# Kernel optimization log

Hardware: AMD Instinct MI355X
Metric: run time of the kernel (lower is better)

Reference implementation:

```python
import jax, jax.numpy as jnp
import numpy as np

B, H, W, Q, E, M, K, WIN = 4, 192, 192, 160, 96, 96, 4, 7
NO_ELECTRON_WEIGHT = 0.1


def _bce_logits(x, z):
    # binary_cross_entropy_with_logits, elementwise: softplus(x) - x*z
    return jnp.logaddexp(0.0, x) - x * z


def setup_inputs() -> dict:
    key = jax.random.key(0)
    ks = jax.random.split(key, 11)
    is_electron_logit = jax.random.normal(ks[0], (B * Q,), jnp.float32)
    true_segmap = jax.random.uniform(ks[1], (B, H, W, E), jnp.float32)
    binary_mask_logits = jax.random.normal(ks[2], (B, H, W, Q), jnp.float32)
    portion_logits = jax.random.normal(ks[3], (B, H, W, Q), jnp.float32)
    # keep incidence points away from borders so the 7x7 window stays in-bounds
    incidence_points = jax.random.uniform(ks[4], (B, E, 2), jnp.float32) * (H - 8) + 4.0
    positions = jax.random.uniform(ks[5], (B, Q, 2), jnp.float32) * H
    a = jax.random.normal(ks[6], (B, Q, 3), jnp.float32)
    l00 = jax.nn.softplus(a[..., 0]) + 0.1
    l11 = jax.nn.softplus(a[..., 2]) + 0.1
    l10 = 0.5 * a[..., 1]
    zero = jnp.zeros_like(l00)
    chol = jnp.stack([jnp.stack([l00, zero], -1), jnp.stack([l10, l11], -1)], -2)  # [B,Q,2,2] lower-tri
    occupancy_logits = jax.random.normal(ks[7], (B, H, W, K), jnp.float32)
    occupancy_true = jax.random.randint(ks[8], (B, H, W), 0, K, jnp.int32)
    qkeys = jax.random.split(ks[9], B)
    matched_q = jnp.stack([jax.random.permutation(k, Q)[:M] for k in qkeys]).astype(jnp.int32)
    ekeys = jax.random.split(ks[10], B)
    matched_e = jnp.stack([jax.random.permutation(k, E) for k in ekeys]).astype(jnp.int32)
    return dict(is_electron_logit=is_electron_logit, true_segmap=true_segmap,
                binary_mask_logits=binary_mask_logits, portion_logits=portion_logits,
                incidence_points=incidence_points, positions=positions, chol=chol,
                occupancy_logits=occupancy_logits, occupancy_true=occupancy_true,
                matched_q=matched_q, matched_e=matched_e)


def reference(is_electron_logit, true_segmap, binary_mask_logits, portion_logits,
              incidence_points, positions, chol, occupancy_logits, occupancy_true,
              matched_q, matched_e):
    # ---- class loss (weighted BCE over flat per-query logits) ----
    labels = jnp.zeros((B * Q,), is_electron_logit.dtype)
    glob = (jnp.arange(B)[:, None] * Q + matched_q).reshape(-1)
    labels = labels.at[glob].set(1.0)
    weights = jnp.where(labels > 0, 1.0, NO_ELECTRON_WEIGHT).astype(is_electron_logit.dtype)
    class_loss = jnp.mean(weights * _bce_logits(is_electron_logit, labels))

    # ---- reorder segmentation maps to matched order (_reorder_segmentation_map) ----
    true_r = jnp.take_along_axis(true_segmap, matched_e[:, None, None, :], axis=3)        # [B,H,W,M]
    bin_r = jnp.take_along_axis(binary_mask_logits, matched_q[:, None, None, :], axis=3)  # [B,H,W,M]
    por_r = jnp.take_along_axis(portion_logits, matched_q[:, None, None, :], axis=3)      # [B,H,W,M]

    # ---- mask BCE on 7x7 windows around floor(matched incidence point) ----
    pts_r = jnp.take_along_axis(incidence_points, matched_e[..., None], axis=1)  # [B,M,2]
    pix = jnp.floor(pts_r).astype(jnp.int32)
    half = WIN // 2
    dr = jnp.arange(-half, half + 1)
    rows = pix[..., 0][:, :, None, None] + dr[None, None, :, None]  # [B,M,7,1]
    cols = pix[..., 1][:, :, None, None] + dr[None, None, None, :]  # [B,M,1,7]
    bi = jnp.arange(B)[:, None, None, None]
    mi = jnp.arange(M)[None, :, None, None]
    tv = true_r[bi, rows, cols, mi]  # [B,M,7,7]
    lg = bin_r[bi, rows, cols, mi]
    bce_loss = jnp.mean(_bce_logits(lg, tv))

    # ---- dice loss (softmax over matched-electron dim) ----
    portion = jax.nn.softmax(por_r, axis=-1)
    num = jnp.sum(2.0 * true_r * portion, axis=(1, 2, 3))
    den = jnp.sum(true_r + portion, axis=(1, 2, 3))
    dice_loss = jnp.mean(1.0 - (num + 1.0) / (den + 1.0))

    # ---- distance NLL (2D MVN with lower-tri scale) ----
    centers_r = jnp.take_along_axis(positions, matched_q[..., None], axis=1)       # [B,M,2]
    chol_r = jnp.take_along_axis(chol, matched_q[..., None, None], axis=1)         # [B,M,2,2]
    d = pts_r - centers_r
    z0 = d[..., 0] / chol_r[..., 0, 0]
    z1 = (d[..., 1] - chol_r[..., 1, 0] * z0) / chol_r[..., 1, 1]
    nll = 0.5 * (z0 * z0 + z1 * z1) + jnp.log(2.0 * jnp.pi) \
          + jnp.log(chol_r[..., 0, 0]) + jnp.log(chol_r[..., 1, 1])
    nll = jnp.where(jnp.isinf(nll), 1e7, nll)
    nll_loss = jnp.mean(nll)

    # ---- occupancy loss (per-pixel electron-count cross-entropy) ----
    logp = jax.nn.log_softmax(occupancy_logits, axis=-1)
    occ_loss = -jnp.mean(jnp.take_along_axis(logp, occupancy_true[..., None], axis=-1))

    # loss_weights all 1.0 (defaults); dot(weights, terms)
    return class_loss + bce_loss + dice_loss + nll_loss + occ_loss
```

## Files before the change

### kernel.cpp

```cpp
#include <hip/hip_runtime.h>
#include <math.h>

#define B_ 4
#define H_ 192
#define W_ 192
#define Q_ 160
#define E_ 96
#define M_ 96
#define HW_ (H_ * W_)
#define NPIX_ (B_ * HW_)
#define TPIX 8
#define TILES_PER_BLK 18
#define NDICE 1024
#define NSMALL 962
#define NBUCKET 64
#define WS_NUM0 4
#define WS_TS0  260
#define WS_TOTAL 516

#define POR_BYTES (TPIX * Q_ * 4)
#define TRU_BYTES (TPIX * E_ * 4)
#define TILE_BYTES (POR_BYTES + TRU_BYTES)
#define POR_F (TPIX * Q_)

__device__ __forceinline__ void stage16(const void* g, void* l) {
    __builtin_amdgcn_global_load_lds(
        (const __attribute__((address_space(1))) void*)g,
        (__attribute__((address_space(3))) void*)l, 16, 0, 0);
}

template <int CTRL, int RMASK>
__device__ __forceinline__ float dpp_add_step(float x) {
    int v = __builtin_amdgcn_update_dpp(0, __float_as_int(x), CTRL, RMASK, 0xF, false);
    return x + __int_as_float(v);
}
__device__ __forceinline__ float wave_sum63(float x) {
    x = dpp_add_step<0x111, 0xF>(x);
    x = dpp_add_step<0x112, 0xF>(x);
    x = dpp_add_step<0x114, 0xF>(x);
    x = dpp_add_step<0x118, 0xF>(x);
    x = dpp_add_step<0x142, 0xA>(x);
    x = dpp_add_step<0x143, 0xC>(x);
    return x;
}

__device__ __forceinline__ float waveSumAll(float v) {
    for (int m = 32; m > 0; m >>= 1) v += __shfl_xor(v, m, 64);
    return v;
}

__device__ __forceinline__ float softplusf(float x) {
    return fmaxf(x, 0.f) + log1pf(__expf(-fabsf(x)));
}

__global__ __launch_bounds__(256) void fused_kernel(
    const float* __restrict__ logit,
    const float* __restrict__ trueseg,
    const float* __restrict__ binlog,
    const float* __restrict__ por,
    const float* __restrict__ inc,
    const float* __restrict__ pos,
    const float* __restrict__ chol,
    const float* __restrict__ occlog,
    const int* __restrict__ occtrue,
    const int* __restrict__ mqall,
    const int* __restrict__ meall,
    float* __restrict__ ws)
{
    __shared__ float tilebuf[2 * TILE_BYTES / 4];
    const int tid  = threadIdx.x;
    const int lane = tid & 63;
    const int wid  = tid >> 6;
    const int blk  = blockIdx.x;

    if (blk < NDICE) {
        const int b = blk >> 8;
        const int slot = blk & 255;
        const bool hi = lane < 32;
        const int* mq = mqall + b * M_;
        const int* me = meall + b * M_;
        const int mqa = mq[lane];
        const int mea = me[lane];
        int mqb = 0, meb = 0;
        if (hi) { mqb = mq[64 + lane]; meb = me[64 + lane]; }
        const char* porb = (const char*)(por + (size_t)b * HW_ * Q_);
        const char* trb  = (const char*)(trueseg + (size_t)b * HW_ * E_);

        float an = 0.f;
        float at = 0.f;

        {
            const int p0 = slot * TPIX;
            const char* gp = porb + (size_t)p0 * (Q_ * 4);
            const char* gt = trb  + (size_t)p0 * (E_ * 4);
            #pragma unroll
            for (int i = 0; i < 2; ++i) {
                const int off = i * 4096 + wid * 1024;
                const char* src = (off < POR_BYTES) ? (gp + off)
                                                    : (gt + (off - POR_BYTES));
                stage16(src + lane * 16, (char*)tilebuf + off);
            }
        }

        int bufsel = 0;
        for (int t = 0; t < TILES_PER_BLK; ++t) {
            __syncthreads();
            if (t + 1 < TILES_PER_BLK) {
                const int p0 = (slot + (t + 1) * 256) * TPIX;
                const char* gp = porb + (size_t)p0 * (Q_ * 4);
                const char* gt = trb  + (size_t)p0 * (E_ * 4);
                const int nb = bufsel ^ 1;
                #pragma unroll
                for (int i = 0; i < 2; ++i) {
                    const int off = i * 4096 + wid * 1024;
                    const char* src = (off < POR_BYTES) ? (gp + off)
                                                        : (gt + (off - POR_BYTES));
                    stage16(src + lane * 16, (char*)tilebuf + nb * TILE_BYTES + off);
                }
            }
            const float* pl = tilebuf + bufsel * (TILE_BYTES / 4);
            const float* tl = pl + POR_F;
            #pragma unroll
            for (int k = 0; k < 2; ++k) {
                const int pix = wid * 2 + k;
                float p0v = pl[pix * Q_ + mqa];
                float t0  = tl[pix * E_ + mea];
                float e1 = 0.f, se1 = 0.f, t1 = 0.f;
                if (hi) {
                    float p1 = pl[pix * Q_ + mqb];
                    t1 = tl[pix * E_ + meb];
                    e1 = __expf(p1);
                    se1 = t1 * e1;
                }
                float e0 = __expf(p0v);
                float s  = wave_sum63(e0 + e1);
                float se = wave_sum63(t0 * e0 + se1);
                an += __fdividef(se, s);
                at += t0 + t1;
            }
            bufsel ^= 1;
        }
        float atr = wave_sum63(at);
        if (lane == 63) {
            int bucket = blk & (NBUCKET - 1);
            atomicAdd(&ws[WS_NUM0 + bucket * 4 + b], 2.f * an);
            atomicAdd(&ws[WS_TS0  + bucket * 4 + b], atr);
        }
    } else {
        float* lab = tilebuf;
        const int s = blk - NDICE;
        float acc = 0.f;
        if (s == 0) {
            for (int i = tid; i < B_ * Q_; i += 256) lab[i] = 0.f;
            __syncthreads();
            for (int i = tid; i < B_ * M_; i += 256) {
                int b = i / M_;
                lab[b * Q_ + mqall[i]] = 1.f;
            }
            __syncthreads();
            for (int i = tid; i < B_ * Q_; i += 256) {
                float x = logit[i];
                float z = lab[i];
                float w = z > 0.f ? 1.f : 0.1f;
                acc += w * (softplusf(x) - x * z);
            }
            float wsum = wave_sum63(acc);
            if (lane == 63) atomicAdd(&ws[0], wsum);
        } else if (s == 1) {
            for (int i = tid; i < B_ * M_; i += 256) {
                int b = i / M_;
                int qi = mqall[i];
                int ei = meall[i];
                float px = inc[(b * E_ + ei) * 2 + 0];
                float py = inc[(b * E_ + ei) * 2 + 1];
                float cx = pos[(b * Q_ + qi) * 2 + 0];
                float cy = pos[(b * Q_ + qi) * 2 + 1];
                const float* ch = chol + (size_t)(b * Q_ + qi) * 4;
                float l00 = ch[0], l10 = ch[2], l11 = ch[3];
                float d0 = px - cx, d1 = py - cy;
                float z0 = d0 / l00;
                float z1 = (d1 - l10 * z0) / l11;
                float nll = 0.5f * (z0 * z0 + z1 * z1) + 1.837877066409345f
                            + logf(l00) + logf(l11);
                if (isinf(nll)) nll = 1e7f;
                acc += nll;
            }
            float wsum = wave_sum63(acc);
            if (lane == 63) atomicAdd(&ws[2], wsum);
        } else if (s < 386) {
            int idx = s - 2;
            int b = idx / M_;
            int ei = meall[idx];
            int qi = mqall[idx];
            float px = inc[(b * E_ + ei) * 2 + 0];
            float py = inc[(b * E_ + ei) * 2 + 1];
            int r0 = (int)floorf(px) - 3;
            int c0 = (int)floorf(py) - 3;
            if (tid < 49) {
                int rr = r0 + tid / 7;
                int cc = c0 + tid % 7;
                size_t pix = ((size_t)b * H_ + rr) * W_ + cc;
                float tv = trueseg[pix * E_ + ei];
                float lg = binlog[pix * Q_ + qi];
                acc = softplusf(lg) - lg * tv;
            }
            if (wid == 0) {
                float wsum = wave_sum63(acc);
                if (lane == 63) atomicAdd(&ws[1], wsum);
            }
        } else {
            int p = (s - 386) * 256 + tid;
            if (p < NPIX_) {
                float4 v = *(const float4*)(occlog + (size_t)p * 4);
                int lb = occtrue[p];
                float m = fmaxf(fmaxf(v.x, v.y), fmaxf(v.z, v.w));
                float lse = m + __logf(__expf(v.x - m) + __expf(v.y - m) +
                                       __expf(v.z - m) + __expf(v.w - m));
                float xs = lb == 0 ? v.x : (lb == 1 ? v.y : (lb == 2 ? v.z : v.w));
                acc = lse - xs;
            }
            float wsum = wave_sum63(acc);
            if (lane == 63) atomicAdd(&ws[3], wsum);
        }
    }
}

__global__ __launch_bounds__(64) void final_kernel(const float* __restrict__ ws,
                                                   float* __restrict__ out)
{
    const int lane = threadIdx.x;
    float n[B_], t[B_];
    for (int b = 0; b < B_; ++b) {
        n[b] = waveSumAll(ws[WS_NUM0 + lane * 4 + b]);
        t[b] = waveSumAll(ws[WS_TS0  + lane * 4 + b]);
    }
    if (lane == 0) {
        float class_l = ws[0] * (1.f / (B_ * Q_));
        float bce_l   = ws[1] * (1.f / (B_ * M_ * 49));
        float nll_l   = ws[2] * (1.f / (B_ * M_));
        float occ_l   = ws[3] * (1.f / NPIX_);
        float dice = 0.f;
        for (int b = 0; b < B_; ++b)
            dice += 1.f - (n[b] + 1.f) / (t[b] + (float)HW_ + 1.f);
        dice *= (1.f / B_);
        out[0] = class_l + bce_l + nll_l + occ_l + dice;
    }
}

extern "C" void kernel_launch(void* const* d_in, const int* in_sizes, int n_in,
                              void* d_out, int out_size, void* d_ws, size_t ws_size,
                              hipStream_t stream) {
    const float* logit   = (const float*)d_in[0];
    const float* trueseg = (const float*)d_in[1];
    const float* binlog  = (const float*)d_in[2];
    const float* por     = (const float*)d_in[3];
    const float* inc     = (const float*)d_in[4];
    const float* pos     = (const float*)d_in[5];
    const float* chol    = (const float*)d_in[6];
    const float* occlog  = (const float*)d_in[7];
    const int*   occtrue = (const int*)d_in[8];
    const int*   mq      = (const int*)d_in[9];
    const int*   me      = (const int*)d_in[10];
    float* out = (float*)d_out;
    float* ws  = (float*)d_ws;

    (void)hipMemsetAsync(d_ws, 0, WS_TOTAL * sizeof(float), stream);

    hipLaunchKernelGGL(fused_kernel, dim3(NDICE + NSMALL), dim3(256), 0, stream,
                       logit, trueseg, binlog, por, inc, pos, chol, occlog, occtrue,
                       mq, me, ws);
    hipLaunchKernelGGL(final_kernel, dim3(1), dim3(64), 0, stream, ws, out);
}
```

Measured before the change: 248.1 us.

## Replace LDS double-buffered tile staging with direct global gathers in dice loop

Measured after the change: 260.2 us. 1.05x slower.

```diff
diff --git a/kernel.cpp b/kernel.cpp
--- a/kernel.cpp
+++ b/kernel.cpp
@@ -10,24 +10,13 @@
 #define HW_ (H_ * W_)
 #define NPIX_ (B_ * HW_)
 #define TPIX 8
-#define TILES_PER_BLK 18
+#define NJOB 36
 #define NDICE 1024
 #define NSMALL 962
 #define NBUCKET 64
 #define WS_NUM0 4
 #define WS_TS0  260
 #define WS_TOTAL 516
-
-#define POR_BYTES (TPIX * Q_ * 4)
-#define TRU_BYTES (TPIX * E_ * 4)
-#define TILE_BYTES (POR_BYTES + TRU_BYTES)
-#define POR_F (TPIX * Q_)
-
-__device__ __forceinline__ void stage16(const void* g, void* l) {
-    __builtin_amdgcn_global_load_lds(
-        (const __attribute__((address_space(1))) void*)g,
-        (__attribute__((address_space(3))) void*)l, 16, 0, 0);
-}
 
 template <int CTRL, int RMASK>
 __device__ __forceinline__ float dpp_add_step(float x) {
@@ -67,7 +56,7 @@
     const int* __restrict__ meall,
     float* __restrict__ ws)
 {
-    __shared__ float tilebuf[2 * TILE_BYTES / 4];
+    __shared__ float lab[B_ * Q_];
     const int tid  = threadIdx.x;
     const int lane = tid & 63;
     const int wid  = tid >> 6;
@@ -83,63 +72,31 @@
         const int mea = me[lane];
         int mqb = 0, meb = 0;
         if (hi) { mqb = mq[64 + lane]; meb = me[64 + lane]; }
-        const char* porb = (const char*)(por + (size_t)b * HW_ * Q_);
-        const char* trb  = (const char*)(trueseg + (size_t)b * HW_ * E_);
+        const float m1 = hi ? 1.f : 0.f;
+
+        const float* porb = por + (size_t)b * HW_ * Q_;
+        const float* trb  = trueseg + (size_t)b * HW_ * E_;
 
         float an = 0.f;
         float at = 0.f;
 
-        {
-            const int p0 = slot * TPIX;
-            const char* gp = porb + (size_t)p0 * (Q_ * 4);
-            const char* gt = trb  + (size_t)p0 * (E_ * 4);
-            #pragma unroll
-            for (int i = 0; i < 2; ++i) {
-                const int off = i * 4096 + wid * 1024;
-                const char* src = (off < POR_BYTES) ? (gp + off)
-                                                    : (gt + (off - POR_BYTES));
-                stage16(src + lane * 16, (char*)tilebuf + off);
-            }
+        #pragma unroll 4
+        for (int j = 0; j < NJOB; ++j) {
+            const int pix = (slot + (j >> 1) * 256) * TPIX + wid * 2 + (j & 1);
+            const float* pr = porb + (size_t)pix * Q_;
+            const float* tr = trb  + (size_t)pix * E_;
+            float p0v = pr[mqa];
+            float t0  = tr[mea];
+            float p1  = pr[mqb];
+            float t1  = tr[meb];
+            float e0 = __expf(p0v);
+            float e1 = __expf(p1) * m1;
+            float s  = wave_sum63(e0 + e1);
+            float se = wave_sum63(fmaf(t1, e1, t0 * e0));
+            an += __fdividef(se, s);
+            at += fmaf(t1, m1, t0);
         }
 
-        int bufsel = 0;
-        for (int t = 0; t < TILES_PER_BLK; ++t) {
-            __syncthreads();
-            if (t + 1 < TILES_PER_BLK) {
-                const int p0 = (slot + (t + 1) * 256) * TPIX;
-                const char* gp = porb + (size_t)p0 * (Q_ * 4);
-                const char* gt = trb  + (size_t)p0 * (E_ * 4);
-                const int nb = bufsel ^ 1;
-                #pragma unroll
-                for (int i = 0; i < 2; ++i) {
-                    const int off = i * 4096 + wid * 1024;
-                    const char* src = (off < POR_BYTES) ? (gp + off)
-                                                        : (gt + (off - POR_BYTES));
-                    stage16(src + lane * 16, (char*)tilebuf + nb * TILE_BYTES + off);
-                }
-            }
-            const float* pl = tilebuf + bufsel * (TILE_BYTES / 4);
-            const float* tl = pl + POR_F;
-            #pragma unroll
-            for (int k = 0; k < 2; ++k) {
-                const int pix = wid * 2 + k;
-                float p0v = pl[pix * Q_ + mqa];
-                float t0  = tl[pix * E_ + mea];
-                float e1 = 0.f, se1 = 0.f, t1 = 0.f;
-                if (hi) {
-                    float p1 = pl[pix * Q_ + mqb];
-                    t1 = tl[pix * E_ + meb];
-                    e1 = __expf(p1);
-                    se1 = t1 * e1;
-                }
-                float e0 = __expf(p0v);
-                float s  = wave_sum63(e0 + e1);
-                float se = wave_sum63(t0 * e0 + se1);
-                an += __fdividef(se, s);
-                at += t0 + t1;
-            }
-            bufsel ^= 1;
-        }
         float atr = wave_sum63(at);
         if (lane == 63) {
             int bucket = blk & (NBUCKET - 1);
@@ -147,7 +104,6 @@
             atomicAdd(&ws[WS_TS0  + bucket * 4 + b], atr);
         }
     } else {
-        float* lab = tilebuf;
         const int s = blk - NDICE;
         float acc = 0.f;
         if (s == 0) {
```
